# Optimization experiments

Hardware: AMD Instinct MI355X
Metric: run time of the kernel (lower is better)

## Reference

```python
import jax, jax.numpy as jnp
import numpy as np

IN_FEATURES = 4096
OUT_FEATURES = 11008
BATCH = 256


def unpack_i4(q):
    # q: [K//2, N] packed bytes; row 2k = low nibble, row 2k+1 = high nibble
    low = q & 15
    high = (q >> 4) & 15
    # interleave -> [K, N]
    return jnp.stack([low, high], axis=1).reshape(q.shape[0] * 2, q.shape[1])


def setup_inputs() -> dict:
    key = jax.random.key(0)
    k1, k2, k3, k4 = jax.random.split(key, 4)
    x = jax.random.normal(k1, (BATCH, IN_FEATURES), dtype=jnp.float32)
    qweight = jax.random.randint(k2, (IN_FEATURES // 2, OUT_FEATURES), 0, 256, dtype=jnp.int32)
    scales = jax.random.uniform(k3, (OUT_FEATURES,), dtype=jnp.float32)
    zeroes = jax.random.normal(k4, (OUT_FEATURES,), dtype=jnp.float32)
    return {"x": x, "qweight": qweight, "scales": scales, "zeroes": zeroes}


def reference(x, qweight, scales, zeroes):
    # Dequantize: per-output-channel scale/zero over unpacked int4 weights
    w = scales[None, :] * unpack_i4(qweight).astype(jnp.float32) - zeroes[None, :]  # [K, N]
    return x @ w  # [B, N]
```

## Files before the change

kernel.cpp:

```cpp
#include <hip/hip_runtime.h>
#include <stdint.h>

#define K_DIM 4096
#define N_DIM 11008
#define M_DIM 256

typedef uint32_t u32;
using frag_ab = __attribute__((ext_vector_type(8))) short;
using frag_cd = __attribute__((ext_vector_type(4))) float;
using u32x2   = __attribute__((ext_vector_type(2))) uint32_t;

typedef __attribute__((address_space(3))) const char lds_cc;

#define DSR128(dst, addr, off)                                       \
    asm volatile("ds_read_b128 %0, %1 offset:" #off                  \
                 : "=&v"(dst) : "v"(addr))
#define DSR2(dst, addr, o0, o1)                                      \
    asm volatile("ds_read2_b32 %0, %1 offset0:" #o0 " offset1:" #o1  \
                 : "=&v"(dst) : "v"(addr))

__device__ __forceinline__ u32 f2bf_rn(float f) {
    u32 u = __builtin_bit_cast(u32, f);
    return (u + 0x7FFFu + ((u >> 16) & 1u)) >> 16;
}
__device__ __forceinline__ float bf2f(u32 b) {
    return __builtin_bit_cast(float, b << 16);
}
__device__ __forceinline__ void gll16(const void* g, void* l) {
    __builtin_amdgcn_global_load_lds(
        (const __attribute__((address_space(1))) u32*)g,
        (__attribute__((address_space(3))) u32*)l, 16, 0, 0);
}

#define BFCVT(q) ((u32)((__mul24((int)(q), 0x4004) & 0x003C003C) | 0x42004200))

__global__ __launch_bounds__(256) void prep_kernel(const float* __restrict__ x,
                                                   ushort* __restrict__ xbf,
                                                   float* __restrict__ rowsum) {
    const int row = blockIdx.x;
    const int tid = threadIdx.x;
    const float* xr = x + (size_t)row * K_DIM;
    ushort* br = xbf + (size_t)row * K_DIM;
    float s = 0.0f;
#pragma unroll
    for (int p = 0; p < 4; ++p) {
        int i = p * 1024 + tid * 4;
        float4 v = *reinterpret_cast<const float4*>(xr + i);
        u32 b0 = f2bf_rn(v.x), b1 = f2bf_rn(v.y), b2 = f2bf_rn(v.z), b3 = f2bf_rn(v.w);
        uint2 o;
        o.x = b0 | (b1 << 16);
        o.y = b2 | (b3 << 16);
        *reinterpret_cast<uint2*>(br + i) = o;
        s += bf2f(b0) + bf2f(b1) + bf2f(b2) + bf2f(b3);
    }
#pragma unroll
    for (int off = 32; off > 0; off >>= 1) s += __shfl_down(s, off, 64);
    __shared__ float wsum[4];
    if ((tid & 63) == 0) wsum[tid >> 6] = s;
    __syncthreads();
    if (tid == 0) rowsum[row] = wsum[0] + wsum[1] + wsum[2] + wsum[3];
}

__global__ __launch_bounds__(256, 4) void gemm_kernel(const int* __restrict__ qw,
                                                      const float* __restrict__ scales,
                                                      const float* __restrict__ zeroes,
                                                      const ushort* __restrict__ xbf,
                                                      const float* __restrict__ rowsum,
                                                      float* __restrict__ out,
                                                      float* __restrict__ partial,
                                                      int split2) {
    __shared__ uint4 Alds[3][512];
    __shared__ u32   Blds[3][1024];

    const u32* qwu = (const u32*)qw;
    const int tid  = threadIdx.x;
    const int lane = tid & 63;
    const int wid  = tid >> 6;
    const int l4   = lane & 15;
    const int c    = lane >> 4;

    const int orig = blockIdx.x;
    int nb, mb, sp, NTt;
    if (split2) {
        int wg = (orig & 7) * 86 + (orig >> 3);
        nb = wg >> 2; mb = (wg >> 1) & 1; sp = wg & 1; NTt = 64;
    } else {
        int wg = (orig & 7) * 43 + (orig >> 3);
        nb = wg >> 1; mb = wg & 1; sp = 0; NTt = 128;
    }
    const int n0 = nb * 64;
    const int m0 = mb * 128;
    const int kb = sp * 64;
    const int wm = wid >> 1;
    const int wn = wid & 1;

    const ushort* asrc[2];
#pragma unroll
    for (int j = 0; j < 2; ++j)
        asrc[j] = xbf + (size_t)(m0 + (wid * 2 + j) * 16 + (lane >> 2)) * K_DIM +
                  8 * ((lane & 3) ^ ((lane >> 3) & 3));
    const u32* bsrc = qwu + (size_t)(wid * 4 + (lane >> 4)) * N_DIM + n0 +
                      4 * ((lane & 15) ^ ((wid & 1) << 2));

    const u32 aoff = (u32)((wm * 64 + l4) * 64 + ((c ^ ((l4 >> 1) & 3)) << 4));
    u32 boffs[2];
#pragma unroll
    for (int nf = 0; nf < 2; ++nf)
        boffs[nf] = (u32)(((c * 4) * 64 +
                           ((wn * 32 + nf * 16 + l4) ^ ((c & 1) << 4))) * 4);

    frag_cd acc[4][2];
#pragma unroll
    for (int i = 0; i < 4; ++i) {
        acc[i][0] = (frag_cd){0.f, 0.f, 0.f, 0.f};
        acc[i][1] = (frag_cd){0.f, 0.f, 0.f, 0.f};
    }

    auto stage = [&](int t_abs, int buf) {
#pragma unroll
        for (int j = 0; j < 2; ++j)
            gll16(asrc[j] + (size_t)t_abs * 32, &Alds[buf][(wid * 2 + j) * 64]);
        gll16(bsrc + (size_t)t_abs * 16 * N_DIM, &Blds[buf][wid * 256]);
    };

    auto compute = [&](int buf) {
        lds_cc* Ab = (lds_cc*)&Alds[buf][0];
        lds_cc* Bb = (lds_cc*)&Blds[buf][0];
        frag_ab afr[4];
        DSR128(afr[0], Ab + aoff, 0);
        DSR128(afr[1], Ab + aoff, 1024);
        DSR128(afr[2], Ab + aoff, 2048);
        DSR128(afr[3], Ab + aoff, 3072);
        u32x2 br[2][2];
        DSR2(br[0][0], Bb + boffs[0], 0, 64);
        DSR2(br[0][1], Bb + boffs[0], 128, 192);
        DSR2(br[1][0], Bb + boffs[1], 0, 64);
        DSR2(br[1][1], Bb + boffs[1], 128, 192);
        asm volatile("s_waitcnt lgkmcnt(0)" ::: "memory");
        __builtin_amdgcn_sched_barrier(0);
#pragma unroll
        for (int nf = 0; nf < 2; ++nf) {
            union { frag_ab f; u32 u[4]; } bb;
            bb.u[0] = BFCVT(br[nf][0][0]);
            bb.u[1] = BFCVT(br[nf][0][1]);
            bb.u[2] = BFCVT(br[nf][1][0]);
            bb.u[3] = BFCVT(br[nf][1][1]);
#pragma unroll
            for (int mf = 0; mf < 4; ++mf)
                acc[mf][nf] = __builtin_amdgcn_mfma_f32_16x16x32_bf16(
                    afr[mf], bb.f, acc[mf][nf], 0, 0, 0);
        }
    };

    stage(kb + 0, 0);
    stage(kb + 1, 1);

    int cur = 0;
    for (int t = 0; t < NTt; ++t) {
        int pbuf = cur + 2; if (pbuf >= 3) pbuf -= 3;
        if (t + 2 < NTt) {
            stage(kb + t + 2, pbuf);
            asm volatile("s_waitcnt vmcnt(6)" ::: "memory");
        } else if (t + 1 < NTt) {
            asm volatile("s_waitcnt vmcnt(3)" ::: "memory");
        } else {
            asm volatile("s_waitcnt vmcnt(0)" ::: "memory");
        }
        __builtin_amdgcn_s_barrier();
        __builtin_amdgcn_sched_barrier(0);
        compute(cur);
        asm volatile("" ::: "memory");
        __builtin_amdgcn_s_barrier();
        ++cur; if (cur >= 3) cur -= 3;
    }

    float sc[2], zp[2];
#pragma unroll
    for (int nf = 0; nf < 2; ++nf) {
        int n = n0 + wn * 32 + nf * 16 + l4;
        sc[nf] = scales[n];
        zp[nf] = zeroes[n] + 32.0f * sc[nf];
    }
    if (sp == 0) {
        float rs[4][4];
#pragma unroll
        for (int mf = 0; mf < 4; ++mf)
#pragma unroll
            for (int j = 0; j < 4; ++j)
                rs[mf][j] = rowsum[m0 + wm * 64 + mf * 16 + c * 4 + j];
#pragma unroll
        for (int mf = 0; mf < 4; ++mf)
#pragma unroll
            for (int nf = 0; nf < 2; ++nf)
#pragma unroll
                for (int j = 0; j < 4; ++j) {
                    int m = m0 + wm * 64 + mf * 16 + c * 4 + j;
                    out[(size_t)m * N_DIM + n0 + wn * 32 + nf * 16 + l4] =
                        sc[nf] * acc[mf][nf][j] - zp[nf] * rs[mf][j];
                }
    } else {
#pragma unroll
        for (int mf = 0; mf < 4; ++mf)
#pragma unroll
            for (int nf = 0; nf < 2; ++nf)
#pragma unroll
                for (int j = 0; j < 4; ++j) {
                    int m = m0 + wm * 64 + mf * 16 + c * 4 + j;
                    partial[(size_t)m * N_DIM + n0 + wn * 32 + nf * 16 + l4] =
                        sc[nf] * acc[mf][nf][j];
                }
    }
}

__global__ __launch_bounds__(256) void reduce_kernel(float* __restrict__ out,
                                                     const float* __restrict__ partial) {
    size_t i = ((size_t)blockIdx.x * 256 + threadIdx.x) * 4;
    float4 o = *reinterpret_cast<float4*>(out + i);
    float4 p = *reinterpret_cast<const float4*>(partial + i);
    o.x += p.x; o.y += p.y; o.z += p.z; o.w += p.w;
    *reinterpret_cast<float4*>(out + i) = o;
}

extern "C" void kernel_launch(void* const* d_in, const int* in_sizes, int n_in,
                              void* d_out, int out_size, void* d_ws, size_t ws_size,
                              hipStream_t stream) {
    const float* x      = (const float*)d_in[0];
    const int*   qw     = (const int*)d_in[1];
    const float* scales = (const float*)d_in[2];
    const float* zeroes = (const float*)d_in[3];
    float* out = (float*)d_out;

    const size_t XBF_BYTES = (size_t)M_DIM * K_DIM * 2;
    const size_t RS_OFF    = XBF_BYTES;
    const size_t P_OFF     = XBF_BYTES + 4096;
    const size_t P_BYTES   = (size_t)M_DIM * N_DIM * 4;

    ushort* xbf    = (ushort*)d_ws;
    float*  rowsum = (float*)((char*)d_ws + RS_OFF);
    float*  part   = (float*)((char*)d_ws + P_OFF);

    const bool split2 = ws_size >= P_OFF + P_BYTES;

    prep_kernel<<<M_DIM, 256, 0, stream>>>(x, xbf, rowsum);
    if (split2) {
        gemm_kernel<<<688, 256, 0, stream>>>(qw, scales, zeroes, xbf, rowsum,
                                             out, part, 1);
        reduce_kernel<<<(M_DIM * N_DIM) / (256 * 4), 256, 0, stream>>>(out, part);
    } else {
        gemm_kernel<<<344, 256, 0, stream>>>(qw, scales, zeroes, xbf, rowsum,
                                             out, nullptr, 0);
    }
}
```

Before: 57.94 us.

## Deepen LDS pipeline to six stages and drop trailing barrier

Doubles the LDS ring from three to six buffers and prefetches four K-tiles ahead instead of two, waiting on vmcnt(12) with a drained tail. The second barrier after each compute is removed, relying on buffer distance to avoid overwriting tiles still being read. Launch bounds drop to 2 waves-per-EU since LDS use doubles (about 72 KB per block), reducing occupancy in exchange for more loads in flight. With the trailing barrier gone, a fast wave could restage a buffer that a slow wave is still reading if the distance is not enough.

New measurement: 61.66 us. 6.4% more time.

```diff
diff --git a/kernel.cpp b/kernel.cpp
--- a/kernel.cpp
+++ b/kernel.cpp
@@ -61,7 +61,7 @@
     if (tid == 0) rowsum[row] = wsum[0] + wsum[1] + wsum[2] + wsum[3];
 }
 
-__global__ __launch_bounds__(256, 4) void gemm_kernel(const int* __restrict__ qw,
+__global__ __launch_bounds__(256, 2) void gemm_kernel(const int* __restrict__ qw,
                                                       const float* __restrict__ scales,
                                                       const float* __restrict__ zeroes,
                                                       const ushort* __restrict__ xbf,
@@ -69,8 +69,8 @@
                                                       float* __restrict__ out,
                                                       float* __restrict__ partial,
                                                       int split2) {
-    __shared__ uint4 Alds[3][512];
-    __shared__ u32   Blds[3][1024];
+    __shared__ uint4 Alds[6][512];
+    __shared__ u32   Blds[6][1024];
 
     const u32* qwu = (const u32*)qw;
     const int tid  = threadIdx.x;
@@ -154,25 +154,30 @@
 
     stage(kb + 0, 0);
     stage(kb + 1, 1);
-
-    int cur = 0;
-    for (int t = 0; t < NTt; ++t) {
-        int pbuf = cur + 2; if (pbuf >= 3) pbuf -= 3;
-        if (t + 2 < NTt) {
-            stage(kb + t + 2, pbuf);
-            asm volatile("s_waitcnt vmcnt(6)" ::: "memory");
-        } else if (t + 1 < NTt) {
-            asm volatile("s_waitcnt vmcnt(3)" ::: "memory");
-        } else {
-            asm volatile("s_waitcnt vmcnt(0)" ::: "memory");
-        }
+    stage(kb + 2, 2);
+    stage(kb + 3, 3);
+
+    int cb = 0, pb = 4;
+    for (int t = 0; t < NTt - 4; ++t) {
+        stage(kb + t + 4, pb);
+        asm volatile("s_waitcnt vmcnt(12)" ::: "memory");
         __builtin_amdgcn_s_barrier();
         __builtin_amdgcn_sched_barrier(0);
-        compute(cur);
-        asm volatile("" ::: "memory");
-        __builtin_amdgcn_s_barrier();
-        ++cur; if (cur >= 3) cur -= 3;
-    }
+        compute(cb);
+        ++cb; if (cb >= 6) cb = 0;
+        ++pb; if (pb >= 6) pb = 0;
+    }
+#define TAILSTEP(W)                                          \
+    asm volatile("s_waitcnt vmcnt(" #W ")" ::: "memory");    \
+    __builtin_amdgcn_s_barrier();                            \
+    __builtin_amdgcn_sched_barrier(0);                       \
+    compute(cb);                                             \
+    ++cb; if (cb >= 6) cb = 0;
+    TAILSTEP(9)
+    TAILSTEP(6)
+    TAILSTEP(3)
+    TAILSTEP(0)
+#undef TAILSTEP
 
     float sc[2], zp[2];
 #pragma unroll
```

## Use full-M 256x128 tiles with 512 threads, split-K by four, bf16 partials

Applied to the files above, without the earlier changes.

The GEMM block grows to 512 threads. Each block now covers all 256 rows and 128 output columns, so B-fragment reads widen to four 16-column groups per wave. K is split four ways instead of two, which keeps enough blocks in the grid, and the three non-leading splits write their partial sums as bf16 into a workspace. The reduce kernel then adds these three partials to the output. The aim is more reuse of dequantized weights per x load and less partial-sum traffic, at the cost of 72KB LDS per block and bf16 rounding in the partials, which may hurt accuracy.

Result: faster. 53.01 us (-8.5%).

```diff
diff --git a/kernel.cpp b/kernel.cpp
--- a/kernel.cpp
+++ b/kernel.cpp
@@ -8,15 +8,14 @@
 typedef uint32_t u32;
 using frag_ab = __attribute__((ext_vector_type(8))) short;
 using frag_cd = __attribute__((ext_vector_type(4))) float;
-using u32x2   = __attribute__((ext_vector_type(2))) uint32_t;
 
 typedef __attribute__((address_space(3))) const char lds_cc;
 
 #define DSR128(dst, addr, off)                                       \
     asm volatile("ds_read_b128 %0, %1 offset:" #off                  \
                  : "=&v"(dst) : "v"(addr))
-#define DSR2(dst, addr, o0, o1)                                      \
-    asm volatile("ds_read2_b32 %0, %1 offset0:" #o0 " offset1:" #o1  \
+#define DSR32(dst, addr, off)                                        \
+    asm volatile("ds_read_b32 %0, %1 offset:" #off                   \
                  : "=&v"(dst) : "v"(addr))
 
 __device__ __forceinline__ u32 f2bf_rn(float f) {
@@ -61,16 +60,16 @@
     if (tid == 0) rowsum[row] = wsum[0] + wsum[1] + wsum[2] + wsum[3];
 }
 
-__global__ __launch_bounds__(256, 4) void gemm_kernel(const int* __restrict__ qw,
+__global__ __launch_bounds__(512, 4) void gemm_kernel(const int* __restrict__ qw,
                                                       const float* __restrict__ scales,
                                                       const float* __restrict__ zeroes,
                                                       const ushort* __restrict__ xbf,
                                                       const float* __restrict__ rowsum,
                                                       float* __restrict__ out,
-                                                      float* __restrict__ partial,
-                                                      int split2) {
-    __shared__ uint4 Alds[3][512];
-    __shared__ u32   Blds[3][1024];
+                                                      ushort* __restrict__ partial,
+                                                      int split4) {
+    __shared__ uint4 Alds[3][1024];
+    __shared__ u32   Blds[3][2048];
 
     const u32* qwu = (const u32*)qw;
     const int tid  = threadIdx.x;
@@ -80,47 +79,41 @@
     const int c    = lane >> 4;
 
     const int orig = blockIdx.x;
-    int nb, mb, sp, NTt;
-    if (split2) {
-        int wg = (orig & 7) * 86 + (orig >> 3);
-        nb = wg >> 2; mb = (wg >> 1) & 1; sp = wg & 1; NTt = 64;
+    int nb, sp, NTt, kb;
+    if (split4) {
+        int wg = (orig & 7) * 43 + (orig >> 3);
+        nb = wg >> 2; sp = wg & 3; NTt = 32; kb = sp * 32;
     } else {
-        int wg = (orig & 7) * 43 + (orig >> 3);
-        nb = wg >> 1; mb = wg & 1; sp = 0; NTt = 128;
-    }
-    const int n0 = nb * 64;
-    const int m0 = mb * 128;
-    const int kb = sp * 64;
+        nb = orig; sp = 0; NTt = 128; kb = 0;
+    }
+    const int n0 = nb * 128;
     const int wm = wid >> 1;
     const int wn = wid & 1;
 
     const ushort* asrc[2];
 #pragma unroll
     for (int j = 0; j < 2; ++j)
-        asrc[j] = xbf + (size_t)(m0 + (wid * 2 + j) * 16 + (lane >> 2)) * K_DIM +
+        asrc[j] = xbf + (size_t)((wid * 2 + j) * 16 + (lane >> 2)) * K_DIM +
                   8 * ((lane & 3) ^ ((lane >> 3) & 3));
-    const u32* bsrc = qwu + (size_t)(wid * 4 + (lane >> 4)) * N_DIM + n0 +
-                      4 * ((lane & 15) ^ ((wid & 1) << 2));
+    const u32* bsrc = qwu + (size_t)(wid * 2 + (lane >> 5)) * N_DIM + n0 +
+                      (((lane & 31) * 4) ^ (((wid >> 1) & 1) << 4));
 
     const u32 aoff = (u32)((wm * 64 + l4) * 64 + ((c ^ ((l4 >> 1) & 3)) << 4));
-    u32 boffs[2];
-#pragma unroll
-    for (int nf = 0; nf < 2; ++nf)
-        boffs[nf] = (u32)(((c * 4) * 64 +
-                           ((wn * 32 + nf * 16 + l4) ^ ((c & 1) << 4))) * 4);
-
-    frag_cd acc[4][2];
-#pragma unroll
-    for (int i = 0; i < 4; ++i) {
-        acc[i][0] = (frag_cd){0.f, 0.f, 0.f, 0.f};
-        acc[i][1] = (frag_cd){0.f, 0.f, 0.f, 0.f};
-    }
-
-    auto stage = [&](int t_abs, int buf) {
+    const u32 b0off = (u32)((c * 512 + wn * 64 + ((c & 1) << 4) + l4) * 4);
+    const u32 b1off = (u32)((c * 512 + wn * 64 + ((1 ^ (c & 1)) << 4) + l4) * 4);
+
+    frag_cd acc[4][4];
+#pragma unroll
+    for (int i = 0; i < 4; ++i)
+#pragma unroll
+        for (int j = 0; j < 4; ++j)
+            acc[i][j] = (frag_cd){0.f, 0.f, 0.f, 0.f};
+
+    auto stage = [&](int t, int buf) {
 #pragma unroll
         for (int j = 0; j < 2; ++j)
-            gll16(asrc[j] + (size_t)t_abs * 32, &Alds[buf][(wid * 2 + j) * 64]);
-        gll16(bsrc + (size_t)t_abs * 16 * N_DIM, &Blds[buf][wid * 256]);
+            gll16(asrc[j] + (size_t)(kb + t) * 32, &Alds[buf][(wid * 2 + j) * 64]);
+        gll16(bsrc + (size_t)(kb + t) * 16 * N_DIM, &Blds[buf][wid * 256]);
     };
 
     auto compute = [&](int buf) {
@@ -131,20 +124,32 @@
         DSR128(afr[1], Ab + aoff, 1024);
         DSR128(afr[2], Ab + aoff, 2048);
         DSR128(afr[3], Ab + aoff, 3072);
-        u32x2 br[2][2];
-        DSR2(br[0][0], Bb + boffs[0], 0, 64);
-        DSR2(br[0][1], Bb + boffs[0], 128, 192);
-        DSR2(br[1][0], Bb + boffs[1], 0, 64);
-        DSR2(br[1][1], Bb + boffs[1], 128, 192);
+        u32 bq[16];
+        DSR32(bq[0],  Bb + b0off, 0);
+        DSR32(bq[1],  Bb + b0off, 512);
+        DSR32(bq[2],  Bb + b0off, 1024);
+        DSR32(bq[3],  Bb + b0off, 1536);
+        DSR32(bq[4],  Bb + b1off, 0);
+        DSR32(bq[5],  Bb + b1off, 512);
+        DSR32(bq[6],  Bb + b1off, 1024);
+        DSR32(bq[7],  Bb + b1off, 1536);
+        DSR32(bq[8],  Bb + b0off, 128);
+        DSR32(bq[9],  Bb + b0off, 640);
+        DSR32(bq[10], Bb + b0off, 1152);
+        DSR32(bq[11], Bb + b0off, 1664);
+        DSR32(bq[12], Bb + b1off, 128);
+        DSR32(bq[13], Bb + b1off, 640);
+        DSR32(bq[14], Bb + b1off, 1152);
+        DSR32(bq[15], Bb + b1off, 1664);
         asm volatile("s_waitcnt lgkmcnt(0)" ::: "memory");
         __builtin_amdgcn_sched_barrier(0);
 #pragma unroll
-        for (int nf = 0; nf < 2; ++nf) {
+        for (int nf = 0; nf < 4; ++nf) {
             union { frag_ab f; u32 u[4]; } bb;
-            bb.u[0] = BFCVT(br[nf][0][0]);
-            bb.u[1] = BFCVT(br[nf][0][1]);
-            bb.u[2] = BFCVT(br[nf][1][0]);
-            bb.u[3] = BFCVT(br[nf][1][1]);
+            bb.u[0] = BFCVT(bq[nf * 4 + 0]);
+            bb.u[1] = BFCVT(bq[nf * 4 + 1]);
+            bb.u[2] = BFCVT(bq[nf * 4 + 2]);
+            bb.u[3] = BFCVT(bq[nf * 4 + 3]);
 #pragma unroll
             for (int mf = 0; mf < 4; ++mf)
                 acc[mf][nf] = __builtin_amdgcn_mfma_f32_16x16x32_bf16(
@@ -152,14 +157,14 @@
         }
     };
 
-    stage(kb + 0, 0);
-    stage(kb + 1, 1);
+    stage(0, 0);
+    stage(1, 1);
 
     int cur = 0;
     for (int t = 0; t < NTt; ++t) {
         int pbuf = cur + 2; if (pbuf >= 3) pbuf -= 3;
         if (t + 2 < NTt) {
-            stage(kb + t + 2, pbuf);
+            stage(t + 2, pbuf);
             asm volatile("s_waitcnt vmcnt(6)" ::: "memory");
         } else if (t + 1 < NTt) {
             asm volatile("s_waitcnt vmcnt(3)" ::: "memory");
@@ -174,10 +179,10 @@
         ++cur; if (cur >= 3) cur -= 3;
     }
 
-    float sc[2], zp[2];
-#pragma unroll
-    for (int nf = 0; nf < 2; ++nf) {
-        int n = n0 + wn * 32 + nf * 16 + l4;
+    float sc[4], zp[4];
+#pragma unroll
+    for (int nf = 0; nf < 4; ++nf) {
+        int n = n0 + wn * 64 + nf * 16 + l4;
         sc[nf] = scales[n];
         zp[nf] = zeroes[n] + 32.0f * sc[nf];
     }
@@ -187,37 +192,44 @@
         for (int mf = 0; mf < 4; ++mf)
 #pragma unroll
             for (int j = 0; j < 4; ++j)
-                rs[mf][j] = rowsum[m0 + wm * 64 + mf * 16 + c * 4 + j];
+                rs[mf][j] = rowsum[wm * 64 + mf * 16 + c * 4 + j];
 #pragma unroll
         for (int mf = 0; mf < 4; ++mf)
 #pragma unroll
-            for (int nf = 0; nf < 2; ++nf)
+            for (int nf = 0; nf < 4; ++nf)
 #pragma unroll
                 for (int j = 0; j < 4; ++j) {
-                    int m = m0 + wm * 64 + mf * 16 + c * 4 + j;
-                    out[(size_t)m * N_DIM + n0 + wn * 32 + nf * 16 + l4] =
+                    int m = wm * 64 + mf * 16 + c * 4 + j;
+                    out[(size_t)m * N_DIM + n0 + wn * 64 + nf * 16 + l4] =
                         sc[nf] * acc[mf][nf][j] - zp[nf] * rs[mf][j];
                 }
     } else {
+        ushort* pb = partial + (size_t)(sp - 1) * M_DIM * N_DIM;
 #pragma unroll
         for (int mf = 0; mf < 4; ++mf)
 #pragma unroll
-            for (int nf = 0; nf < 2; ++nf)
+            for (int nf = 0; nf < 4; ++nf)
 #pragma unroll
                 for (int j = 0; j < 4; ++j) {
-                    int m = m0 + wm * 64 + mf * 16 + c * 4 + j;
-                    partial[(size_t)m * N_DIM + n0 + wn * 32 + nf * 16 + l4] =
-                        sc[nf] * acc[mf][nf][j];
+                    int m = wm * 64 + mf * 16 + c * 4 + j;
+                    pb[(size_t)m * N_DIM + n0 + wn * 64 + nf * 16 + l4] =
+                        (ushort)f2bf_rn(sc[nf] * acc[mf][nf][j]);
                 }
     }
 }
 
 __global__ __launch_bounds__(256) void reduce_kernel(float* __restrict__ out,
-                                                     const float* __restrict__ partial) {
+                                                     const ushort* __restrict__ partial) {
+    const size_t NTOT = (size_t)M_DIM * N_DIM;
     size_t i = ((size_t)blockIdx.x * 256 + threadIdx.x) * 4;
     float4 o = *reinterpret_cast<float4*>(out + i);
-    float4 p = *reinterpret_cast<const float4*>(partial + i);
-    o.x += p.x; o.y += p.y; o.z += p.z; o.w += p.w;
+    ushort4 a = *reinterpret_cast<const ushort4*>(partial + i);
+    ushort4 b = *reinterpret_cast<const ushort4*>(partial + NTOT + i);
+    ushort4 d = *reinterpret_cast<const ushort4*>(partial + 2 * NTOT + i);
+    o.x += bf2f(a.x) + bf2f(b.x) + bf2f(d.x);
+    o.y += bf2f(a.y) + bf2f(b.y) + bf2f(d.y);
+    o.z += bf2f(a.z) + bf2f(b.z) + bf2f(d.z);
+    o.w += bf2f(a.w) + bf2f(b.w) + bf2f(d.w);
     *reinterpret_cast<float4*>(out + i) = o;
 }
 
@@ -233,21 +245,21 @@
     const size_t XBF_BYTES = (size_t)M_DIM * K_DIM * 2;
     const size_t RS_OFF    = XBF_BYTES;
     const size_t P_OFF     = XBF_BYTES + 4096;
-    const size_t P_BYTES   = (size_t)M_DIM * N_DIM * 4;
+    const size_t P_BYTES   = (size_t)3 * M_DIM * N_DIM * 2;
 
     ushort* xbf    = (ushort*)d_ws;
     float*  rowsum = (float*)((char*)d_ws + RS_OFF);
-    float*  part   = (float*)((char*)d_ws + P_OFF);
-
-    const bool split2 = ws_size >= P_OFF + P_BYTES;
+    ushort* part   = (ushort*)((char*)d_ws + P_OFF);
+
+    const bool split4 = ws_size >= P_OFF + P_BYTES;
 
     prep_kernel<<<M_DIM, 256, 0, stream>>>(x, xbf, rowsum);
-    if (split2) {
-        gemm_kernel<<<688, 256, 0, stream>>>(qw, scales, zeroes, xbf, rowsum,
+    if (split4) {
+        gemm_kernel<<<344, 512, 0, stream>>>(qw, scales, zeroes, xbf, rowsum,
                                              out, part, 1);
         reduce_kernel<<<(M_DIM * N_DIM) / (256 * 4), 256, 0, stream>>>(out, part);
     } else {
-        gemm_kernel<<<344, 256, 0, stream>>>(qw, scales, zeroes, xbf, rowsum,
-                                             out, nullptr, 0);
-    }
-}
+        gemm_kernel<<<86, 512, 0, stream>>>(qw, scales, zeroes, xbf, rowsum,
+                                            out, nullptr, 0);
+    }
+}
```
